# Optimization experiments

Hardware: AMD Instinct MI355X
Metric: run time of the kernel (lower is better)

The kernel has to match this reference:

```python
import jax, jax.numpy as jnp
import numpy as np

V, D, T, L, H = 32000, 1024, 2048, 2, 16
HS = D // H  # per-head dim (head_size // nheads)
FF = 4 * D
EPS = 1e-5


def _ln(x, g, b):
    m = jnp.mean(x, axis=-1, keepdims=True)
    v = jnp.mean((x - m) ** 2, axis=-1, keepdims=True)
    return (x - m) * jax.lax.rsqrt(v + EPS) * g + b


def setup_inputs() -> dict:
    key = jax.random.key(0)
    ks = jax.random.split(key, 16)
    s = lambda k, shape, fan: jax.random.normal(k, shape, jnp.float32) * (fan ** -0.5)
    return {
        "inputs": jax.random.randint(ks[0], (1, T), 0, V, dtype=jnp.int64),
        "tok_emb": s(ks[1], (V, D), D),
        "pos_emb": s(ks[2], (T, D), D),
        "ln1_g": jnp.ones((L, D)), "ln1_b": jnp.zeros((L, D)),
        "wq": s(ks[3], (L, H, D, HS), D),
        "wk": s(ks[4], (L, H, D, HS), D),
        "wv": s(ks[5], (L, H, D, HS), D),
        "ln2_g": jnp.ones((L, D)), "ln2_b": jnp.zeros((L, D)),
        "w1": s(ks[6], (L, D, FF), D), "b1": jnp.zeros((L, FF)),
        "w2": s(ks[7], (L, FF, D), FF), "b2": jnp.zeros((L, D)),
        "lnf_g": jnp.ones((D,)), "lnf_b": jnp.zeros((D,)),
        "w_un": s(ks[8], (D, V), D), "b_un": jnp.zeros((V,)),
    }


def reference(inputs, tok_emb, pos_emb, ln1_g, ln1_b, wq, wk, wv,
              ln2_g, ln2_b, w1, b1, w2, b2, lnf_g, lnf_b, w_un, b_un):
    b, t = inputs.shape
    x = tok_emb[inputs] + pos_emb[:t]  # [B,T,D]
    mask = jnp.tril(jnp.ones((t, t), dtype=bool))
    scale = jnp.asarray(D, x.dtype) ** -0.5  # source scales by x.shape[-1]**-0.5
    neg_inf = jnp.asarray(-jnp.inf, x.dtype)
    for l in range(L):
        h = _ln(x, ln1_g[l], ln1_b[l])
        q = jnp.einsum('btc,hcs->bhts', h, wq[l])
        k = jnp.einsum('btc,hcs->bhts', h, wk[l])
        v = jnp.einsum('btc,hcs->bhts', h, wv[l])
        scores = jnp.einsum('bhts,bhus->bhtu', q, k) * scale  # [B,H,T,T]
        scores = jnp.where(mask, scores, neg_inf)
        p = jax.nn.softmax(scores, axis=-1)
        att = jnp.einsum('bhtu,bhus->bhts', p, v)  # [B,H,T,HS]
        att = att.transpose(0, 2, 1, 3).reshape(b, t, H * HS)
        x = x + att
        h = _ln(x, ln2_g[l], ln2_b[l])
        h = jax.nn.relu(h @ w1[l] + b1[l]) @ w2[l] + b2[l]
        x = x + h
    x = _ln(x, lnf_g, lnf_b)
    return x @ w_un + b_un  # [B,T,V]
```

## Files before the change

### kernel.cpp

```cpp
#include <hip/hip_runtime.h>
#include <hip/hip_bf16.h>

#define TT 2048
#define DD 1024
#define NH 16
#define HSZ 64
#define FFD 4096
#define VV 32000
#define NL 2

typedef __bf16 bf16x8 __attribute__((ext_vector_type(8)));
typedef float f32x4 __attribute__((ext_vector_type(4)));

__device__ __forceinline__ unsigned short f2bf(float f) {
    unsigned int u = __float_as_uint(f);
    return (unsigned short)((u + 0x7FFFu + ((u >> 16) & 1u)) >> 16);
}

#define GLL(gsrc, ldst) \
  __builtin_amdgcn_global_load_lds((const __attribute__((address_space(1))) void*)(gsrc), \
                                   (__attribute__((address_space(3))) void*)(ldst), 16, 0, 0)

#define SWZ64(L)  ((L) ^ ((((L) >> 7) & 3) << 4))
#define SWZ128(L) ((L) ^ ((((L) >> 7) & 7) << 4))
#define SWZ256(L) ((L) ^ ((((L) >> 8) & 7) << 4))

#define VMW(n) asm volatile("s_waitcnt vmcnt(" #n ")" ::: "memory")

__global__ __launch_bounds__(256) void embed_ln(
    const int* __restrict__ idx, const float* __restrict__ tok,
    const float* __restrict__ pos, const float* __restrict__ g,
    const float* __restrict__ b, float* __restrict__ x,
    unsigned short* __restrict__ h)
{
    int t = blockIdx.x;
    int tid = threadIdx.x;
    int d4 = tid * 4;
    int token = idx[t];
    float4 a = *(const float4*)&tok[(size_t)token * DD + d4];
    float4 p = *(const float4*)&pos[(size_t)t * DD + d4];
    float4 xv;
    xv.x = a.x + p.x; xv.y = a.y + p.y; xv.z = a.z + p.z; xv.w = a.w + p.w;
    *(float4*)&x[(size_t)t * DD + d4] = xv;
    float s  = xv.x + xv.y + xv.z + xv.w;
    float s2 = xv.x*xv.x + xv.y*xv.y + xv.z*xv.z + xv.w*xv.w;
    #pragma unroll
    for (int off = 32; off >= 1; off >>= 1) {
        s  += __shfl_xor(s,  off);
        s2 += __shfl_xor(s2, off);
    }
    __shared__ float ls[4], ls2[4];
    int w = tid >> 6;
    if ((tid & 63) == 0) { ls[w] = s; ls2[w] = s2; }
    __syncthreads();
    float sum  = ls[0] + ls[1] + ls[2] + ls[3];
    float sum2 = ls2[0] + ls2[1] + ls2[2] + ls2[3];
    float mean = sum * (1.0f / DD);
    float var  = sum2 * (1.0f / DD) - mean * mean;
    float r = rsqrtf(var + 1e-5f);
    float4 gv = *(const float4*)&g[d4];
    float4 bv = *(const float4*)&b[d4];
    ushort4 pk;
    pk.x = f2bf((xv.x - mean) * r * gv.x + bv.x);
    pk.y = f2bf((xv.y - mean) * r * gv.y + bv.y);
    pk.z = f2bf((xv.z - mean) * r * gv.z + bv.z);
    pk.w = f2bf((xv.w - mean) * r * gv.w + bv.w);
    *(ushort4*)&h[(size_t)t * DD + d4] = pk;
}

__global__ __launch_bounds__(256) void ln_kernel(
    const float* __restrict__ x, const float* __restrict__ g,
    const float* __restrict__ b, unsigned short* __restrict__ out)
{
    int t = blockIdx.x;
    int tid = threadIdx.x;
    int d4 = tid * 4;
    float4 xv = *(const float4*)&x[(size_t)t * DD + d4];
    float s  = xv.x + xv.y + xv.z + xv.w;
    float s2 = xv.x*xv.x + xv.y*xv.y + xv.z*xv.z + xv.w*xv.w;
    #pragma unroll
    for (int off = 32; off >= 1; off >>= 1) {
        s  += __shfl_xor(s,  off);
        s2 += __shfl_xor(s2, off);
    }
    __shared__ float ls[4], ls2[4];
    int w = tid >> 6;
    if ((tid & 63) == 0) { ls[w] = s; ls2[w] = s2; }
    __syncthreads();
    float sum  = ls[0] + ls[1] + ls[2] + ls[3];
    float sum2 = ls2[0] + ls2[1] + ls2[2] + ls2[3];
    float mean = sum * (1.0f / DD);
    float var  = sum2 * (1.0f / DD) - mean * mean;
    float r = rsqrtf(var + 1e-5f);
    float4 gv = *(const float4*)&g[d4];
    float4 bv = *(const float4*)&b[d4];
    ushort4 pk;
    pk.x = f2bf((xv.x - mean) * r * gv.x + bv.x);
    pk.y = f2bf((xv.y - mean) * r * gv.y + bv.y);
    pk.z = f2bf((xv.z - mean) * r * gv.z + bv.z);
    pk.w = f2bf((xv.w - mean) * r * gv.w + bv.w);
    *(ushort4*)&out[(size_t)t * DD + d4] = pk;
}

__global__ __launch_bounds__(256) void tcast(
    const float* __restrict__ src, unsigned short* __restrict__ dst,
    int R, int C, size_t sstride, size_t dstride)
{
    __shared__ float tile[64][65];
    const float* s = src + (size_t)blockIdx.z * sstride;
    unsigned short* d = dst + (size_t)blockIdx.z * dstride;
    int c0 = blockIdx.x * 64, r0 = blockIdx.y * 64;
    #pragma unroll
    for (int i = 0; i < 16; ++i) {
        int id = i * 256 + threadIdx.x;
        int rr = id >> 6, cc = id & 63;
        tile[rr][cc] = s[(size_t)(r0 + rr) * C + (c0 + cc)];
    }
    __syncthreads();
    #pragma unroll
    for (int i = 0; i < 16; ++i) {
        int id = i * 256 + threadIdx.x;
        int cc = id >> 6, rr = id & 63;
        d[(size_t)(c0 + cc) * R + (r0 + rr)] = f2bf(tile[rr][cc]);
    }
}

__global__ __launch_bounds__(256) void qkv_tcast(
    const float* __restrict__ wq, const float* __restrict__ wk,
    const float* __restrict__ wv, unsigned short* __restrict__ dst)
{
    __shared__ float tile[64][65];
    int l = blockIdx.z;
    int mat = blockIdx.y >> 4, hh = blockIdx.y & 15;
    const float* s = (mat == 0) ? wq : (mat == 1) ? wk : wv;
    s += (((size_t)l * NH + hh) * DD) * HSZ;
    int r0 = blockIdx.x * 64;
    #pragma unroll
    for (int i = 0; i < 16; ++i) {
        int id = i * 256 + threadIdx.x;
        int rr = id >> 6, cc = id & 63;
        tile[rr][cc] = s[(size_t)(r0 + rr) * HSZ + cc];
    }
    __syncthreads();
    unsigned short* d = dst + (size_t)l * 3072 * DD + ((size_t)mat * DD + hh * HSZ) * DD;
    #pragma unroll
    for (int i = 0; i < 16; ++i) {
        int id = i * 256 + threadIdx.x;
        int cc = id >> 6, rr = id & 63;
        d[(size_t)cc * DD + (r0 + rr)] = f2bf(tile[rr][cc]);
    }
}

template<int EPI, int BN>
__global__ __launch_bounds__(256) void mgemm(
    const unsigned short* __restrict__ A, const unsigned short* __restrict__ Bt,
    const float* __restrict__ bias, void* __restrict__ outp,
    int M, int N, int K, int Kst)
{
    constexpr int FN = BN / 64 * 2;
    __shared__ unsigned short As[3][128 * 32];
    __shared__ unsigned short Bs[3][BN * 32];
    int tid = threadIdx.x;
    int w = tid >> 6, lane = tid & 63;
    int l15 = lane & 15, l4 = lane >> 4;
    int bm = blockIdx.y * 128, bn = blockIdx.x * BN;
    int wr = (w >> 1) * 64, wc = (w & 1) * (BN / 2);
    if (EPI == 3) {
        int z = blockIdx.z;
        A  += (size_t)z * K;
        Bt += (size_t)z * K;
        outp = (float*)outp + (size_t)z * TT * DD;
    }

    f32x4 zz = {0.f, 0.f, 0.f, 0.f};
    f32x4 acc[4][FN];
    #pragma unroll
    for (int m = 0; m < 4; ++m)
        #pragma unroll
        for (int n = 0; n < FN; ++n) acc[m][n] = zz;

    int t16 = tid * 16;
    int lg = SWZ64(t16);
    int srow = lg >> 6;
    int skel = (lg & 63) >> 1;
    const unsigned short* aS0 = A + (size_t)(bm + srow) * Kst + skel;
    const unsigned short* aS1 = A + (size_t)(bm + 64 + srow) * Kst + skel;
    const unsigned short* bS0 = Bt + (size_t)(bn + srow) * Kst + skel;
    const unsigned short* bS1 = Bt + (size_t)(bn + 64 + srow) * Kst + skel;

    #define STAGE(t, slot) do { int kk_ = (t) * 32; \
        GLL(aS0 + kk_, (char*)As[slot] + w * 1024); \
        GLL(aS1 + kk_, (char*)As[slot] + 4096 + w * 1024); \
        GLL(bS0 + kk_, (char*)Bs[slot] + w * 1024); \
        if (BN == 128) GLL(bS1 + kk_, (char*)Bs[slot] + 4096 + w * 1024); } while (0)

    int aoff[4], boff[FN];
    #pragma unroll
    for (int m = 0; m < 4; ++m)
        aoff[m] = SWZ64((wr + m * 16 + l15) * 64 + l4 * 16);
    #pragma unroll
    for (int n = 0; n < FN; ++n)
        boff[n] = SWZ64((wc + n * 16 + l15) * 64 + l4 * 16);

    int nt = K >> 5;
    STAGE(0, 0);
    STAGE(1, 1);
    STAGE(2, 2);
    int slot = 0;
    for (int t = 0; t < nt; ++t) {
        if (BN == 128) {
            if (t + 2 < nt)      VMW(8);
            else if (t + 1 < nt) VMW(4);
            else                 VMW(0);
        } else {
            if (t + 2 < nt)      VMW(6);
            else if (t + 1 < nt) VMW(3);
            else                 VMW(0);
        }
        __builtin_amdgcn_sched_barrier(0);
        __builtin_amdgcn_s_barrier();
        __builtin_amdgcn_sched_barrier(0);
        bf16x8 af[4], bfr[FN];
        #pragma unroll
        for (int m = 0; m < 4; ++m) af[m] = *(const bf16x8*)((const char*)As[slot] + aoff[m]);
        #pragma unroll
        for (int n = 0; n < FN; ++n) bfr[n] = *(const bf16x8*)((const char*)Bs[slot] + boff[n]);
        #pragma unroll
        for (int m = 0; m < 4; ++m)
            #pragma unroll
            for (int n = 0; n < FN; ++n)
                acc[m][n] = __builtin_amdgcn_mfma_f32_16x16x32_bf16(af[m], bfr[n], acc[m][n], 0, 0, 0);
        __builtin_amdgcn_sched_barrier(0);
        __builtin_amdgcn_s_barrier();
        __builtin_amdgcn_sched_barrier(0);
        if (t + 3 < nt) STAGE(t + 3, slot);
        slot = (slot == 2) ? 0 : slot + 1;
    }
    #undef STAGE

    #pragma unroll
    for (int m = 0; m < 4; ++m) {
        int row0 = bm + wr + m * 16 + l4 * 4;
        #pragma unroll
        for (int n = 0; n < FN; ++n) {
            int col = bn + wc + n * 16 + l15;
            f32x4 v = acc[m][n];
            if (EPI == 0) {
                int mat = col >> 10, hh = (col >> 6) & 15, ss = col & 63;
                unsigned short* base = (unsigned short*)outp + (size_t)mat * ((size_t)NH * TT * HSZ);
                if (mat < 2) {
                    #pragma unroll
                    for (int i = 0; i < 4; ++i)
                        base[((size_t)hh * TT + row0 + i) * HSZ + ss] = f2bf(v[i]);
                } else {
                    ushort4 pk;
                    pk.x = f2bf(v[0]); pk.y = f2bf(v[1]); pk.z = f2bf(v[2]); pk.w = f2bf(v[3]);
                    *(ushort4*)&base[((size_t)hh * HSZ + ss) * TT + row0] = pk;
                }
            } else if (EPI == 1) {
                float bb = bias[col];
                unsigned short* o = (unsigned short*)outp;
                #pragma unroll
                for (int i = 0; i < 4; ++i)
                    o[(size_t)(row0 + i) * FFD + col] = f2bf(fmaxf(v[i] + bb, 0.f));
            } else if (EPI == 2) {
                float bb = bias[col];
                float* xx = (float*)outp;
                #pragma unroll
                for (int i = 0; i < 4; ++i)
                    xx[(size_t)(row0 + i) * DD + col] += v[i] + bb;
            } else {
                float* xx = (float*)outp;
                #pragma unroll
                for (int i = 0; i < 4; ++i)
                    xx[(size_t)(row0 + i) * DD + col] = v[i];
            }
        }
    }
}

__global__ __launch_bounds__(256) void ffn2_reduce_ln(
    const float* __restrict__ P, const float* __restrict__ b2,
    float* __restrict__ x, const float* __restrict__ g,
    const float* __restrict__ b, unsigned short* __restrict__ h)
{
    int t = blockIdx.x;
    int tid = threadIdx.x;
    int d4 = tid * 4;
    size_t o = (size_t)t * DD + d4;
    float4 p0 = *(const float4*)&P[o];
    float4 p1 = *(const float4*)&P[o + (size_t)TT * DD];
    float4 bb = *(const float4*)&b2[d4];
    float4 xv = *(float4*)&x[o];
    xv.x += p0.x + p1.x + bb.x;
    xv.y += p0.y + p1.y + bb.y;
    xv.z += p0.z + p1.z + bb.z;
    xv.w += p0.w + p1.w + bb.w;
    *(float4*)&x[o] = xv;
    float s  = xv.x + xv.y + xv.z + xv.w;
    float s2 = xv.x*xv.x + xv.y*xv.y + xv.z*xv.z + xv.w*xv.w;
    #pragma unroll
    for (int off = 32; off >= 1; off >>= 1) {
        s  += __shfl_xor(s,  off);
        s2 += __shfl_xor(s2, off);
    }
    __shared__ float ls[4], ls2[4];
    int w = tid >> 6;
    if ((tid & 63) == 0) { ls[w] = s; ls2[w] = s2; }
    __syncthreads();
    float sum  = ls[0] + ls[1] + ls[2] + ls[3];
    float sum2 = ls2[0] + ls2[1] + ls2[2] + ls2[3];
    float mean = sum * (1.0f / DD);
    float var  = sum2 * (1.0f / DD) - mean * mean;
    float r = rsqrtf(var + 1e-5f);
    float4 gv = *(const float4*)&g[d4];
    float4 bv = *(const float4*)&b[d4];
    ushort4 pk;
    pk.x = f2bf((xv.x - mean) * r * gv.x + bv.x);
    pk.y = f2bf((xv.y - mean) * r * gv.y + bv.y);
    pk.z = f2bf((xv.z - mean) * r * gv.z + bv.z);
    pk.w = f2bf((xv.w - mean) * r * gv.w + bv.w);
    *(ushort4*)&h[o] = pk;
}

__global__ __launch_bounds__(512, 2) void mgemm256(
    const unsigned short* __restrict__ A, const unsigned short* __restrict__ Bt,
    const float* __restrict__ bias, float* __restrict__ outp,
    int M, int N, int K)
{
    __shared__ unsigned short As[2][2][128 * 64];
    __shared__ unsigned short Bs[2][2][128 * 64];
    int tid = threadIdx.x;
    int w = tid >> 6, lane = tid & 63;
    int l15 = lane & 15, l4 = lane >> 4;
    int wr = w >> 2, wc = w & 3;
    int bid = blockIdx.x;
    int xcd = bid & 7, j = bid >> 3;
    int mt = j & 7, p = xcd * 16 + (j >> 3);
    if (p >= N / 256) return;
    int bm = mt * 256, bn = p * 256;

    f32x4 zz = {0.f, 0.f, 0.f, 0.f};
    f32x4 acc[8][4];
    #pragma unroll
    for (int m = 0; m < 8; ++m)
        #pragma unroll
        for (int n = 0; n < 4; ++n) acc[m][n] = zz;

    int L0 = w * 1024 + lane * 16;
    int Ls = SWZ128(L0);
    int srow = Ls >> 7;
    int skel = (Ls & 127) >> 1;
    const unsigned short* aS[2], *bS[2];
    aS[0] = A + (size_t)(bm + srow) * K + skel;
    aS[1] = A + (size_t)(bm + 128 + srow) * K + skel;
    bS[0] = Bt + (size_t)(bn + srow) * K + skel;
    bS[1] = Bt + (size_t)(bn + 128 + srow) * K + skel;
    size_t g1 = (size_t)64 * K;

    #define STAGE6(t, buf) do { int kk_ = (t) * 64; \
        GLL(aS[0] + kk_,      (char*)As[buf][0] + w * 1024); \
        GLL(aS[0] + g1 + kk_, (char*)As[buf][0] + 8192 + w * 1024); \
        GLL(aS[1] + kk_,      (char*)As[buf][1] + w * 1024); \
        GLL(aS[1] + g1 + kk_, (char*)As[buf][1] + 8192 + w * 1024); \
        GLL(bS[0] + kk_,      (char*)Bs[buf][0] + w * 1024); \
        GLL(bS[0] + g1 + kk_, (char*)Bs[buf][0] + 8192 + w * 1024); \
        GLL(bS[1] + kk_,      (char*)Bs[buf][1] + w * 1024); \
        GLL(bS[1] + g1 + kk_, (char*)Bs[buf][1] + 8192 + w * 1024); } while (0)

    int aoff[8][2], boff[4][2];
    #pragma unroll
    for (int m = 0; m < 8; ++m)
        #pragma unroll
        for (int ks = 0; ks < 2; ++ks) {
            int La = (m * 16 + l15) * 128 + ks * 64 + l4 * 16;
            aoff[m][ks] = SWZ128(La);
        }
    #pragma unroll
    for (int n = 0; n < 4; ++n)
        #pragma unroll
        for (int ks = 0; ks < 2; ++ks) {
            int Lb = ((wc & 1) * 64 + n * 16 + l15) * 128 + ks * 64 + l4 * 16;
            boff[n][ks] = SWZ128(Lb);
        }

    int nt = K >> 6;
    STAGE6(0, 0);
    STAGE6(1, 1);
    for (int t = 0; t < nt; ++t) {
        int buf = t & 1;
        if (t + 1 < nt) VMW(8);
        else            VMW(0);
        __builtin_amdgcn_sched_barrier(0);
        __builtin_amdgcn_s_barrier();
        __builtin_amdgcn_sched_barrier(0);
        const char* ab = (const char*)As[buf][wr];
        const char* bb = (const char*)Bs[buf][wc >> 1];
        bf16x8 bfr[4][2];
        #pragma unroll
        for (int n = 0; n < 4; ++n)
            #pragma unroll
            for (int ks = 0; ks < 2; ++ks)
                bfr[n][ks] = *(const bf16x8*)(bb + boff[n][ks]);
        __builtin_amdgcn_s_setprio(1);
        #pragma unroll
        for (int rh = 0; rh < 2; ++rh) {
            bf16x8 af[4][2];
            #pragma unroll
            for (int mm = 0; mm < 4; ++mm)
                #pragma unroll
                for (int ks = 0; ks < 2; ++ks)
                    af[mm][ks] = *(const bf16x8*)(ab + aoff[rh * 4 + mm][ks]);
            #pragma unroll
            for (int mm = 0; mm < 4; ++mm)
                #pragma unroll
                for (int n = 0; n < 4; ++n) {
                    acc[rh*4+mm][n] = __builtin_amdgcn_mfma_f32_16x16x32_bf16(af[mm][0], bfr[n][0], acc[rh*4+mm][n], 0, 0, 0);
                    acc[rh*4+mm][n] = __builtin_amdgcn_mfma_f32_16x16x32_bf16(af[mm][1], bfr[n][1], acc[rh*4+mm][n], 0, 0, 0);
                }
        }
        __builtin_amdgcn_s_setprio(0);
        __builtin_amdgcn_sched_barrier(0);
        __builtin_amdgcn_s_barrier();
        __builtin_amdgcn_sched_barrier(0);
        if (t + 2 < nt) STAGE6(t + 2, buf);
    }
    #undef STAGE6

    #pragma unroll
    for (int m = 0; m < 8; ++m) {
        int row0 = bm + wr * 128 + m * 16 + l4 * 4;
        #pragma unroll
        for (int n = 0; n < 4; ++n) {
            int col = bn + wc * 64 + n * 16 + l15;
            float bb = bias[col];
            f32x4 v = acc[m][n];
            #pragma unroll
            for (int i = 0; i < 4; ++i)
                outp[(size_t)(row0 + i) * VV + col] = v[i] + bb;
        }
    }
}

__global__ __launch_bounds__(256) void attn_kernel(
    const unsigned short* __restrict__ qg, const unsigned short* __restrict__ kg,
    const unsigned short* __restrict__ vt, float* __restrict__ x)
{
    __shared__ unsigned short Ks[2][128 * 64];
    __shared__ unsigned short Vs[2][64 * 128];
    __shared__ unsigned short Ps[4][16 * 128];
    int tid = threadIdx.x;
    int w = tid >> 6, lane = tid & 63;
    int l15 = lane & 15, l4 = lane >> 4;
    int bid = blockIdx.x;
    int j = bid >> 3;
    int hh = (bid & 7) * 2 + (j & 1);
    int qb = (31 - (j >> 1)) * 64;

    const unsigned short* qrow = qg + ((size_t)hh * TT + qb + w * 16 + l15) * HSZ + l4 * 8;
    bf16x8 qf0 = *(const bf16x8*)(qrow);
    bf16x8 qf1 = *(const bf16x8*)(qrow + 32);

    int Lu = tid * 16;
    int Lk = SWZ128(Lu);
    int kr = Lk >> 7, kb = Lk & 127;
    int Lv = SWZ256(Lu);
    int vr = Lv >> 8, vb = Lv & 255;
    const char* kbase = (const char*)(kg + (size_t)hh * TT * HSZ);
    const char* vbase = (const char*)(vt + (size_t)hh * HSZ * TT);

    #define ASTAGE(ib, buf) do { \
        int ub_ = (ib) * 128; \
        _Pragma("unroll") \
        for (int g_ = 0; g_ < 4; ++g_) \
            GLL(kbase + (size_t)(ub_ + g_ * 32 + kr) * 128 + kb, \
                (char*)Ks[buf] + g_ * 4096 + tid * 16); \
        _Pragma("unroll") \
        for (int g_ = 0; g_ < 4; ++g_) \
            GLL(vbase + (size_t)(g_ * 16 + vr) * (TT * 2) + (size_t)ub_ * 2 + vb, \
                (char*)Vs[buf] + g_ * 4096 + tid * 16); \
    } while (0)

    f32x4 zz = {0.f, 0.f, 0.f, 0.f};
    f32x4 o[4];
    #pragma unroll
    for (int i = 0; i < 4; ++i) o[i] = zz;
    float mrun = -INFINITY, lrun = 0.f;

    const float scale = 0.03125f;
    int nkv = (qb >> 7) + 1;
    ASTAGE(0, 0);
    if (nkv > 1) ASTAGE(1, 1);
    int cur = 0;
    for (int ib = 0; ib < nkv; ++ib) {
        int ub = ib * 128;
        bool diag = (ub + 128 > qb);
        if (ib + 1 < nkv) VMW(8);
        else              VMW(0);
        __builtin_amdgcn_sched_barrier(0);
        __builtin_amdgcn_s_barrier();
        __builtin_amdgcn_sched_barrier(0);
        const char* ksc = (const char*)Ks[cur];
        const char* vsc = (const char*)Vs[cur];

        f32x4 sfr[8];
        __builtin_amdgcn_s_setprio(1);
        #pragma unroll
        for (int f = 0; f < 8; ++f) {
            int lgb = (f * 16 + l15) * 128 + l4 * 16;
            bf16x8 k0 = *(const bf16x8*)(ksc + SWZ128(lgb));
            bf16x8 k1 = *(const bf16x8*)(ksc + SWZ128(lgb + 64));
            f32x4 z = zz;
            z = __builtin_amdgcn_mfma_f32_16x16x32_bf16(k0, qf0, z, 0, 0, 0);
            z = __builtin_amdgcn_mfma_f32_16x16x32_bf16(k1, qf1, z, 0, 0, 0);
            sfr[f] = z;
        }
        __builtin_amdgcn_s_setprio(0);

        int qrel = qb - ub + w * 16 + l15;
        float mx = -INFINITY;
        #pragma unroll
        for (int f = 0; f < 8; ++f)
            #pragma unroll
            for (int i = 0; i < 4; ++i) {
                float s = sfr[f][i] * scale;
                if (diag && (16 * f + (l4 << 2) + i) > qrel) s = -INFINITY;
                sfr[f][i] = s;
                mx = fmaxf(mx, s);
            }
        mx = fmaxf(mx, __shfl_xor(mx, 16));
        mx = fmaxf(mx, __shfl_xor(mx, 32));
        bool grow = __any(mx > mrun + 8.0f);
        float c = 1.0f;
        if (grow) {
            float mn = fmaxf(mrun, mx);
            c = __expf(mrun - mn);
            mrun = mn;
        }
        float ps = 0.f;
        #pragma unroll
        for (int f = 0; f < 8; ++f)
            #pragma unroll
            for (int i = 0; i < 4; ++i) {
                float p = __expf(sfr[f][i] - mrun);
                sfr[f][i] = p;
                ps += p;
            }
        ps += __shfl_xor(ps, 16);
        ps += __shfl_xor(ps, 32);
        lrun = lrun * c + ps;
        if (grow) {
            #pragma unroll
            for (int i = 0; i < 4; ++i) {
                float ci = __shfl(c, (lane & 48) + (l4 << 2) + i);
                #pragma unroll
                for (int sf = 0; sf < 4; ++sf) o[sf][i] *= ci;
            }
        }

        unsigned short* pw = Ps[w];
        #pragma unroll
        for (int f = 0; f < 8; ++f) {
            unsigned a0 = ((unsigned)f2bf(sfr[f][0])) | (((unsigned)f2bf(sfr[f][1])) << 16);
            unsigned a1 = ((unsigned)f2bf(sfr[f][2])) | (((unsigned)f2bf(sfr[f][3])) << 16);
            int byte0 = l15 * 256 + f * 32 + l4 * 8;
            *(unsigned*)((char*)pw + SWZ256(byte0)) = a0;
            *(unsigned*)((char*)pw + SWZ256(byte0 + 4)) = a1;
        }
        bf16x8 pa[4];
        #pragma unroll
        for (int ks = 0; ks < 4; ++ks)
            pa[ks] = *(const bf16x8*)((const char*)pw + SWZ256(l15 * 256 + ks * 64 + l4 * 16));
        __builtin_amdgcn_s_setprio(1);
        #pragma unroll
        for (int sf = 0; sf < 4; ++sf) {
            f32x4 a = o[sf];
            #pragma unroll
            for (int ks = 0; ks < 4; ++ks) {
                bf16x8 v = *(const bf16x8*)(vsc + SWZ256((sf * 16 + l15) * 256 + ks * 64 + l4 * 16));
                a = __builtin_amdgcn_mfma_f32_16x16x32_bf16(pa[ks], v, a, 0, 0, 0);
            }
            o[sf] = a;
        }
        __builtin_amdgcn_s_setprio(0);
        __builtin_amdgcn_sched_barrier(0);
        __builtin_amdgcn_s_barrier();
        __builtin_amdgcn_sched_barrier(0);
        if (ib + 2 < nkv) ASTAGE(ib + 2, cur);
        cur ^= 1;
    }
    #undef ASTAGE
    float rl[4];
    #pragma unroll
    for (int i = 0; i < 4; ++i)
        rl[i] = 1.0f / __shfl(lrun, (lane & 48) + (l4 << 2) + i);
    #pragma unroll
    for (int sf = 0; sf < 4; ++sf)
        #pragma unroll
        for (int i = 0; i < 4; ++i) {
            int q = qb + w * 16 + l4 * 4 + i;
            int d = hh * HSZ + sf * 16 + l15;
            x[(size_t)q * DD + d] += o[sf][i] * rl[i];
        }
}

extern "C" void kernel_launch(void* const* d_in, const int* in_sizes, int n_in,
                              void* d_out, int out_size, void* d_ws, size_t ws_size,
                              hipStream_t stream)
{
    const int*   idx    = (const int*)  d_in[0];
    const float* tok    = (const float*)d_in[1];
    const float* pos    = (const float*)d_in[2];
    const float* ln1_g  = (const float*)d_in[3];
    const float* ln1_b  = (const float*)d_in[4];
    const float* wq     = (const float*)d_in[5];
    const float* wk     = (const float*)d_in[6];
    const float* wv     = (const float*)d_in[7];
    const float* ln2_g  = (const float*)d_in[8];
    const float* ln2_b  = (const float*)d_in[9];
    const float* w1     = (const float*)d_in[10];
    const float* b1     = (const float*)d_in[11];
    const float* w2     = (const float*)d_in[12];
    const float* b2     = (const float*)d_in[13];
    const float* lnf_g  = (const float*)d_in[14];
    const float* lnf_b  = (const float*)d_in[15];
    const float* w_un   = (const float*)d_in[16];
    const float* b_un   = (const float*)d_in[17];
    float* out = (float*)d_out;

    char* W = (char*)d_ws;
    float*          x    = (float*)(W);
    unsigned short* h    = (unsigned short*)(W + 8388608);
    unsigned short* qg   = (unsigned short*)(W + 12582912);
    unsigned short* kg   = (unsigned short*)(W + 16777216);
    unsigned short* vt   = (unsigned short*)(W + 20971520);
    float*          Pp   = (float*)(W + 8388608);
    unsigned short* h1   = (unsigned short*)(W + 25165824);
    unsigned short* wqkvT= (unsigned short*)(W + 41943040);
    unsigned short* w1T  = (unsigned short*)(W + 54525952);
    unsigned short* w2T  = (unsigned short*)(W + 71303168);
    unsigned short* wunT = (unsigned short*)(W + 88080384);
    (void)kg; (void)ws_size; (void)in_sizes; (void)n_in; (void)out_size;

    qkv_tcast<<<dim3(16, 48, 2), 256, 0, stream>>>(wq, wk, wv, wqkvT);
    tcast<<<dim3(64, 16, 2), 256, 0, stream>>>(w1, w1T, DD, FFD, (size_t)DD * FFD, (size_t)DD * FFD);
    tcast<<<dim3(16, 64, 2), 256, 0, stream>>>(w2, w2T, FFD, DD, (size_t)FFD * DD, (size_t)FFD * DD);
    tcast<<<dim3(500, 16, 1), 256, 0, stream>>>(w_un, wunT, DD, VV, 0, 0);

    embed_ln<<<TT, 256, 0, stream>>>(idx, tok, pos, ln1_g, ln1_b, x, h);

    for (int l = 0; l < NL; ++l) {
        mgemm<0, 64><<<dim3(48, 16), 256, 0, stream>>>(h, wqkvT + (size_t)l * 3072 * DD, nullptr, qg, TT, 3072, DD, DD);
        attn_kernel<<<512, 256, 0, stream>>>(qg, kg, vt, x);
        ln_kernel<<<TT, 256, 0, stream>>>(x, ln2_g + l * DD, ln2_b + l * DD, h);
        mgemm<1, 128><<<dim3(32, 16), 256, 0, stream>>>(h, w1T + (size_t)l * FFD * DD, b1 + (size_t)l * FFD, h1, TT, FFD, DD, DD);
        mgemm<3, 64><<<dim3(16, 16, 2), 256, 0, stream>>>(h1, w2T + (size_t)l * DD * FFD, nullptr, Pp, TT, DD, FFD / 2, FFD);
        const float* ng = (l + 1 < NL) ? (ln1_g + (l + 1) * DD) : lnf_g;
        const float* nb = (l + 1 < NL) ? (ln1_b + (l + 1) * DD) : lnf_b;
        ffn2_reduce_ln<<<TT, 256, 0, stream>>>(Pp, b2 + (size_t)l * DD, x, ng, nb, h);
    }

    mgemm256<<<dim3(1024), 512, 0, stream>>>(h, wunT, b_un, out, TT, VV, DD);
}
```

Baseline: 592.8 us.

## Use 1024-thread unembed GEMM blocks and exp2-based softmax with diagonal skip

The unembedding GEMM now runs 16 waves per block instead of 8, with a 4x4 accumulator tile per wave rather than 8x4. This halves per-wave register pressure and the number of LDS staging loads per thread, while keeping the shared tiles double buffered. In attention, the softmax folds log2(e) into the scale and uses a native exp2 instruction, with the rescale threshold adjusted to match. It also skips exponentials for fully masked 16-column fragments on diagonal blocks. The trade-off is a single block per CU for the GEMM and extra branching in the softmax loop.

```diff
diff --git a/kernel.cpp b/kernel.cpp
--- a/kernel.cpp
+++ b/kernel.cpp
@@ -15,6 +15,14 @@
 __device__ __forceinline__ unsigned short f2bf(float f) {
     unsigned int u = __float_as_uint(f);
     return (unsigned short)((u + 0x7FFFu + ((u >> 16) & 1u)) >> 16);
+}
+
+__device__ __forceinline__ float exp2fast(float x) {
+#if __has_builtin(__builtin_amdgcn_exp2f)
+    return __builtin_amdgcn_exp2f(x);
+#else
+    float r; asm("v_exp_f32 %0, %1" : "=v"(r) : "v"(x)); return r;
+#endif
 }
 
 #define GLL(gsrc, ldst) \
@@ -323,13 +331,13 @@
     *(ushort4*)&h[o] = pk;
 }
 
-__global__ __launch_bounds__(512, 2) void mgemm256(
+__global__ __launch_bounds__(1024, 1) void mgemm256(
     const unsigned short* __restrict__ A, const unsigned short* __restrict__ Bt,
     const float* __restrict__ bias, float* __restrict__ outp,
     int M, int N, int K)
 {
-    __shared__ unsigned short As[2][2][128 * 64];
-    __shared__ unsigned short Bs[2][2][128 * 64];
+    __shared__ unsigned short As[2][256 * 64];
+    __shared__ unsigned short Bs[2][256 * 64];
     int tid = threadIdx.x;
     int w = tid >> 6, lane = tid & 63;
     int l15 = lane & 15, l4 = lane >> 4;
@@ -341,61 +349,50 @@
     int bm = mt * 256, bn = p * 256;
 
     f32x4 zz = {0.f, 0.f, 0.f, 0.f};
-    f32x4 acc[8][4];
-    #pragma unroll
-    for (int m = 0; m < 8; ++m)
+    f32x4 acc[4][4];
+    #pragma unroll
+    for (int m = 0; m < 4; ++m)
         #pragma unroll
         for (int n = 0; n < 4; ++n) acc[m][n] = zz;
 
-    int L0 = w * 1024 + lane * 16;
-    int Ls = SWZ128(L0);
-    int srow = Ls >> 7;
-    int skel = (Ls & 127) >> 1;
-    const unsigned short* aS[2], *bS[2];
-    aS[0] = A + (size_t)(bm + srow) * K + skel;
-    aS[1] = A + (size_t)(bm + 128 + srow) * K + skel;
-    bS[0] = Bt + (size_t)(bn + srow) * K + skel;
-    bS[1] = Bt + (size_t)(bn + 128 + srow) * K + skel;
-    size_t g1 = (size_t)64 * K;
-
-    #define STAGE6(t, buf) do { int kk_ = (t) * 64; \
-        GLL(aS[0] + kk_,      (char*)As[buf][0] + w * 1024); \
-        GLL(aS[0] + g1 + kk_, (char*)As[buf][0] + 8192 + w * 1024); \
-        GLL(aS[1] + kk_,      (char*)As[buf][1] + w * 1024); \
-        GLL(aS[1] + g1 + kk_, (char*)As[buf][1] + 8192 + w * 1024); \
-        GLL(bS[0] + kk_,      (char*)Bs[buf][0] + w * 1024); \
-        GLL(bS[0] + g1 + kk_, (char*)Bs[buf][0] + 8192 + w * 1024); \
-        GLL(bS[1] + kk_,      (char*)Bs[buf][1] + w * 1024); \
-        GLL(bS[1] + g1 + kk_, (char*)Bs[buf][1] + 8192 + w * 1024); } while (0)
-
-    int aoff[8][2], boff[4][2];
-    #pragma unroll
-    for (int m = 0; m < 8; ++m)
-        #pragma unroll
-        for (int ks = 0; ks < 2; ++ks) {
-            int La = (m * 16 + l15) * 128 + ks * 64 + l4 * 16;
-            aoff[m][ks] = SWZ128(La);
-        }
+    int L0 = tid * 16;
+    int srow = L0 >> 7;
+    int skel = (SWZ128(L0) & 127) >> 1;
+    const unsigned short* aS0 = A + (size_t)(bm + srow) * K + skel;
+    const unsigned short* aS1 = A + (size_t)(bm + 128 + srow) * K + skel;
+    const unsigned short* bS0 = Bt + (size_t)(bn + srow) * K + skel;
+    const unsigned short* bS1 = Bt + (size_t)(bn + 128 + srow) * K + skel;
+
+    #define STG(t, buf) do { int kk_ = (t) * 64; \
+        GLL(aS0 + kk_, (char*)As[buf] + w * 1024); \
+        GLL(aS1 + kk_, (char*)As[buf] + 16384 + w * 1024); \
+        GLL(bS0 + kk_, (char*)Bs[buf] + w * 1024); \
+        GLL(bS1 + kk_, (char*)Bs[buf] + 16384 + w * 1024); } while (0)
+
+    int aoff[4][2], boff[4][2];
+    #pragma unroll
+    for (int m = 0; m < 4; ++m)
+        #pragma unroll
+        for (int ks = 0; ks < 2; ++ks)
+            aoff[m][ks] = SWZ128((wr * 64 + m * 16 + l15) * 128 + ks * 64 + l4 * 16);
     #pragma unroll
     for (int n = 0; n < 4; ++n)
         #pragma unroll
-        for (int ks = 0; ks < 2; ++ks) {
-            int Lb = ((wc & 1) * 64 + n * 16 + l15) * 128 + ks * 64 + l4 * 16;
-            boff[n][ks] = SWZ128(Lb);
-        }
+        for (int ks = 0; ks < 2; ++ks)
+            boff[n][ks] = SWZ128((wc * 64 + n * 16 + l15) * 128 + ks * 64 + l4 * 16);
 
     int nt = K >> 6;
-    STAGE6(0, 0);
-    STAGE6(1, 1);
+    STG(0, 0);
+    STG(1, 1);
     for (int t = 0; t < nt; ++t) {
         int buf = t & 1;
-        if (t + 1 < nt) VMW(8);
+        if (t + 1 < nt) VMW(4);
         else            VMW(0);
         __builtin_amdgcn_sched_barrier(0);
         __builtin_amdgcn_s_barrier();
         __builtin_amdgcn_sched_barrier(0);
-        const char* ab = (const char*)As[buf][wr];
-        const char* bb = (const char*)Bs[buf][wc >> 1];
+        const char* ab = (const char*)As[buf];
+        const char* bb = (const char*)Bs[buf];
         bf16x8 bfr[4][2];
         #pragma unroll
         for (int n = 0; n < 4; ++n)
@@ -404,32 +401,26 @@
                 bfr[n][ks] = *(const bf16x8*)(bb + boff[n][ks]);
         __builtin_amdgcn_s_setprio(1);
         #pragma unroll
-        for (int rh = 0; rh < 2; ++rh) {
-            bf16x8 af[4][2];
+        for (int m = 0; m < 4; ++m) {
+            bf16x8 a0 = *(const bf16x8*)(ab + aoff[m][0]);
+            bf16x8 a1 = *(const bf16x8*)(ab + aoff[m][1]);
             #pragma unroll
-            for (int mm = 0; mm < 4; ++mm)
-                #pragma unroll
-                for (int ks = 0; ks < 2; ++ks)
-                    af[mm][ks] = *(const bf16x8*)(ab + aoff[rh * 4 + mm][ks]);
-            #pragma unroll
-            for (int mm = 0; mm < 4; ++mm)
-                #pragma unroll
-                for (int n = 0; n < 4; ++n) {
-                    acc[rh*4+mm][n] = __builtin_amdgcn_mfma_f32_16x16x32_bf16(af[mm][0], bfr[n][0], acc[rh*4+mm][n], 0, 0, 0);
-                    acc[rh*4+mm][n] = __builtin_amdgcn_mfma_f32_16x16x32_bf16(af[mm][1], bfr[n][1], acc[rh*4+mm][n], 0, 0, 0);
-                }
+            for (int n = 0; n < 4; ++n) {
+                acc[m][n] = __builtin_amdgcn_mfma_f32_16x16x32_bf16(a0, bfr[n][0], acc[m][n], 0, 0, 0);
+                acc[m][n] = __builtin_amdgcn_mfma_f32_16x16x32_bf16(a1, bfr[n][1], acc[m][n], 0, 0, 0);
+            }
         }
         __builtin_amdgcn_s_setprio(0);
         __builtin_amdgcn_sched_barrier(0);
         __builtin_amdgcn_s_barrier();
         __builtin_amdgcn_sched_barrier(0);
-        if (t + 2 < nt) STAGE6(t + 2, buf);
-    }
-    #undef STAGE6
-
-    #pragma unroll
-    for (int m = 0; m < 8; ++m) {
-        int row0 = bm + wr * 128 + m * 16 + l4 * 4;
+        if (t + 2 < nt) STG(t + 2, buf);
+    }
+    #undef STG
+
+    #pragma unroll
+    for (int m = 0; m < 4; ++m) {
+        int row0 = bm + wr * 64 + m * 16 + l4 * 4;
         #pragma unroll
         for (int n = 0; n < 4; ++n) {
             int col = bn + wc * 64 + n * 16 + l15;
@@ -487,7 +478,7 @@
     for (int i = 0; i < 4; ++i) o[i] = zz;
     float mrun = -INFINITY, lrun = 0.f;
 
-    const float scale = 0.03125f;
+    const float C2 = 0.03125f * 1.44269504089f;
     int nkv = (qb >> 7) + 1;
     ASTAGE(0, 0);
     if (nkv > 1) ASTAGE(1, 1);
@@ -518,34 +509,41 @@
         __builtin_amdgcn_s_setprio(0);
 
         int qrel = qb - ub + w * 16 + l15;
+        int flive = diag ? ((qb - ub + w * 16 + 15) >> 4) : 7;
         float mx = -INFINITY;
         #pragma unroll
         for (int f = 0; f < 8; ++f)
             #pragma unroll
             for (int i = 0; i < 4; ++i) {
-                float s = sfr[f][i] * scale;
+                float s = sfr[f][i] * C2;
                 if (diag && (16 * f + (l4 << 2) + i) > qrel) s = -INFINITY;
                 sfr[f][i] = s;
                 mx = fmaxf(mx, s);
             }
         mx = fmaxf(mx, __shfl_xor(mx, 16));
         mx = fmaxf(mx, __shfl_xor(mx, 32));
-        bool grow = __any(mx > mrun + 8.0f);
+        bool grow = __any(mx > mrun + 11.5416f);
         float c = 1.0f;
         if (grow) {
             float mn = fmaxf(mrun, mx);
-            c = __expf(mrun - mn);
+            c = exp2fast(mrun - mn);
             mrun = mn;
         }
         float ps = 0.f;
         #pragma unroll
-        for (int f = 0; f < 8; ++f)
-            #pragma unroll
-            for (int i = 0; i < 4; ++i) {
-                float p = __expf(sfr[f][i] - mrun);
-                sfr[f][i] = p;
-                ps += p;
+        for (int f = 0; f < 8; ++f) {
+            if (f <= flive) {
+                #pragma unroll
+                for (int i = 0; i < 4; ++i) {
+                    float p = exp2fast(sfr[f][i] - mrun);
+                    sfr[f][i] = p;
+                    ps += p;
+                }
+            } else {
+                #pragma unroll
+                for (int i = 0; i < 4; ++i) sfr[f][i] = 0.f;
             }
+        }
         ps += __shfl_xor(ps, 16);
         ps += __shfl_xor(ps, 32);
         lrun = lrun * c + ps;
@@ -660,5 +658,5 @@
         ffn2_reduce_ln<<<TT, 256, 0, stream>>>(Pp, b2 + (size_t)l * DD, x, ng, nb, h);
     }
 
-    mgemm256<<<dim3(1024), 512, 0, stream>>>(h, wunT, b_un, out, TT, VV, DD);
-}
+    mgemm256<<<dim3(1024), 1024, 0, stream>>>(h, wunT, b_un, out, TT, VV, DD);
+}
```

Result: slower. 611.2 us (+3.1%).
